# Optimization experiments

Hardware: AMD Instinct MI355X
Metric: run time of the kernel (lower is better)

Reference implementation:

```python
import jax, jax.numpy as jnp
import numpy as np

GROUPS = 32
EPS = 1e-5


def group_norm(x, scale, bias):
    # x: [b, v, t, s, f]; normalize per (b,v,t) sample over (channels_in_group, s)
    b, v, t, s, f = x.shape
    xg = x.reshape(b, v, t, s, GROUPS, f // GROUPS)
    mean = xg.mean(axis=(3, 5), keepdims=True)
    var = xg.var(axis=(3, 5), keepdims=True)
    xn = ((xg - mean) * jax.lax.rsqrt(var + EPS)).reshape(b, v, t, s, f)
    return xn * scale + bias


def nh_conv(x, adjc, W, b):
    # x: [b,v,t,s,f_in]; adjc: [s, k]; W: [k, f_in, f_out]; b: [f_out]
    x_nh = x[:, :, :, adjc, :]                      # [b,v,t,s,k,f_in]
    return jnp.einsum('bvtskf,kfo->bvtso', x_nh, W) + b


def setup_inputs() -> dict:
    key = jax.random.key(0)
    ks = jax.random.split(key, 12)
    B, V, T, S, F_IN, F_OUT, K = 1, 2, 2, 12288, 128, 256, 9
    x = jax.random.normal(ks[0], (B, V, T, S, F_IN), dtype=jnp.float32)
    adjc = jax.random.randint(ks[1], (S, K), 0, S, dtype=jnp.int32)
    gn1_scale = jnp.ones((F_IN,), jnp.float32)
    gn1_bias = jnp.zeros((F_IN,), jnp.float32)
    gn2_scale = jnp.ones((F_OUT,), jnp.float32)
    gn2_bias = jnp.zeros((F_OUT,), jnp.float32)
    W_skip = jax.random.normal(ks[2], (F_IN, F_OUT), jnp.float32) / np.sqrt(F_IN)
    b_skip = jnp.zeros((F_OUT,), jnp.float32)
    W1 = jax.random.normal(ks[3], (K, F_IN, F_OUT), jnp.float32) / np.sqrt(K * F_IN)
    b1 = jnp.zeros((F_OUT,), jnp.float32)
    W2 = jax.random.normal(ks[4], (K, F_OUT, F_OUT), jnp.float32) / np.sqrt(K * F_OUT)
    b2 = jnp.zeros((F_OUT,), jnp.float32)
    return dict(x=x, adjc=adjc, gn1_scale=gn1_scale, gn1_bias=gn1_bias,
                gn2_scale=gn2_scale, gn2_bias=gn2_bias, W_skip=W_skip, b_skip=b_skip,
                W1=W1, b1=b1, W2=W2, b2=b2)


def reference(x, gn1_scale, gn1_bias, gn2_scale, gn2_bias, W_skip, b_skip,
              W1, b1, W2, b2, adjc):
    # skip_layer: ProjLayer with zoom_diff=0 -> plain Linear in->out
    x_res = jnp.einsum('bvtsf,fo->bvtso', x, W_skip) + b_skip
    # norm1 + SiLU (updownconv is Identity when zooms match and in==in feats)
    h = jax.nn.silu(group_norm(x, gn1_scale, gn1_bias))
    # conv1: neighbor-gather linear [k, f_in] -> f_out
    h = nh_conv(h, adjc, W1, b1)
    # emb_layer = Identity; norm2 + SiLU
    h = jax.nn.silu(group_norm(h, gn2_scale, gn2_bias))
    # conv2 + residual
    h = nh_conv(h, adjc, W2, b2)
    return h + x_res
```

## Files before the change

kernel.cpp:

```cpp
#include <hip/hip_runtime.h>
#include <hip/hip_bf16.h>

typedef __bf16 bf16_t;
typedef __bf16 bf16x8 __attribute__((ext_vector_type(8)));
typedef float f32x4 __attribute__((ext_vector_type(4)));
typedef int i32x4 __attribute__((ext_vector_type(4)));

#define S_TOT 12288
#define F_IN 128
#define F_OUT 256
#define EPS 1e-5f

static __device__ __forceinline__ float silu_f(float v) {
  return v / (1.0f + __expf(-v));
}

static __device__ __forceinline__ void gll16(const bf16_t* g, bf16_t* l) {
  __builtin_amdgcn_global_load_lds(
      (const __attribute__((address_space(1))) void*)(const void*)g,
      (__attribute__((address_space(3))) void*)(void*)l, 16, 0, 0);
}

__global__ void prep_kernel(const float* __restrict__ W1,
                            const float* __restrict__ W2,
                            const float* __restrict__ Wsk,
                            bf16_t* __restrict__ W1p,
                            bf16_t* __restrict__ W2p,
                            bf16_t* __restrict__ Wsp,
                            const float* __restrict__ x,
                            float* __restrict__ sum1, float* __restrict__ ss1) {
  __shared__ float gs[32], gq[32];
  if (blockIdx.x < 448) {
    int w = blockIdx.x * 4 + (threadIdx.x >> 6);
    int l = threadIdx.x & 63;
    int lo = l & 15, hi = l >> 4;
    const float* src;
    bf16_t* dst;
    int fbase, obase;
    if (w < 576) {
      int k = w >> 6, rem = w & 63, kc = rem >> 4, cb = rem & 15;
      src = W1 + k * 32768;
      dst = W1p + (size_t)w * 512;
      fbase = 32 * kc + 8 * hi; obase = 16 * cb + lo;
    } else if (w < 1728) {
      int idx = w - 576;
      int k = idx >> 7, rem = idx & 127, kc = rem >> 4, cb = rem & 15;
      src = W2 + k * 65536;
      dst = W2p + (size_t)idx * 512;
      fbase = 32 * kc + 8 * hi; obase = 16 * cb + lo;
    } else {
      int idx = w - 1728;
      int kc = idx >> 4, cb = idx & 15;
      src = Wsk;
      dst = Wsp + (size_t)idx * 512;
      fbase = 32 * kc + 8 * hi; obase = 16 * cb + lo;
    }
    bf16x8 v;
#pragma unroll
    for (int j = 0; j < 8; ++j)
      v[j] = (bf16_t)src[(fbase + j) * 256 + obase];
    *(bf16x8*)(dst + l * 8) = v;
  } else {
    int blk = blockIdx.x - 448;
    int vt = blk & 3;
    int s0 = (blk >> 2) * 256;
    int t = threadIdx.x;
    int col = t & 31, ro = t >> 5;
    float s_ = 0.f, q_ = 0.f;
    const f32x4* xp = (const f32x4*)(x + ((size_t)vt * S_TOT + s0) * F_IN);
#pragma unroll 4
    for (int it = 0; it < 32; ++it) {
      f32x4 v = xp[(size_t)(it * 8 + ro) * 32 + col];
      s_ += v[0] + v[1] + v[2] + v[3];
      q_ += v[0]*v[0] + v[1]*v[1] + v[2]*v[2] + v[3]*v[3];
    }
    if (t < 32) { gs[t] = 0.f; gq[t] = 0.f; }
    __syncthreads();
    atomicAdd(&gs[col], s_);
    atomicAdd(&gq[col], q_);
    __syncthreads();
    if (t < 32) {
      atomicAdd(&sum1[vt * 32 + t], gs[t]);
      atomicAdd(&ss1[vt * 32 + t], gq[t]);
    }
  }
}

__global__ void apply_gn1(const float* __restrict__ x,
                          const float* __restrict__ sum1, const float* __restrict__ ss1,
                          const float* __restrict__ gs, const float* __restrict__ gb,
                          bf16_t* __restrict__ h1) {
  size_t base = ((size_t)blockIdx.x * 256 + threadIdx.x) * 8;
  int vt = (int)(base / ((size_t)S_TOT * F_IN));
  int c0 = (int)(base & (F_IN - 1));
  const f32x4* xp = (const f32x4*)(x + base);
  f32x4 v0 = xp[0], v1 = xp[1];
  float N = (float)(S_TOT * 4);
  bf16x8 o;
#pragma unroll
  for (int gi = 0; gi < 2; ++gi) {
    int g = (c0 >> 2) + gi;
    float mean = sum1[vt * 32 + g] / N;
    float var = ss1[vt * 32 + g] / N - mean * mean;
    float r = rsqrtf(var + EPS);
    f32x4 v = gi ? v1 : v0;
#pragma unroll
    for (int j = 0; j < 4; ++j) {
      int c = g * 4 + j;
      float a = r * gs[c];
      float b = gb[c] - mean * a;
      o[gi * 4 + j] = (bf16_t)silu_f(v[j] * a + b);
    }
  }
  *(bf16x8*)(h1 + base) = o;
}

__global__ void apply_gn2(bf16_t* __restrict__ h,
                          const float* __restrict__ sum_c, const float* __restrict__ ss_c,
                          const float* __restrict__ gs, const float* __restrict__ gb) {
  size_t base = ((size_t)blockIdx.x * 256 + threadIdx.x) * 8;
  int vt = (int)(base / ((size_t)S_TOT * F_OUT));
  int c0 = (int)(base & (F_OUT - 1));
  int g = c0 >> 3;
  bf16x8 v = *(const bf16x8*)(h + base);
  float sg = 0.f, qg = 0.f;
#pragma unroll
  for (int j = 0; j < 8; ++j) {
    sg += sum_c[vt * 256 + g * 8 + j];
    qg += ss_c[vt * 256 + g * 8 + j];
  }
  float N = (float)(S_TOT * 8);
  float mean = sg / N;
  float var = qg / N - mean * mean;
  float r = rsqrtf(var + EPS);
  bf16x8 o;
#pragma unroll
  for (int j = 0; j < 8; ++j) {
    int c = g * 8 + j;
    float a = r * gs[c];
    float b = gb[c] - mean * a;
    o[j] = (bf16_t)silu_f((float)v[j] * a + b);
  }
  *(bf16x8*)(h + base) = o;
}

template<int RE, int NSUB, bool XSK>
__global__ __launch_bounds__(256, 2) void conv_kernel(
    const bf16_t* __restrict__ hsrc, const bf16_t* __restrict__ Wp,
    const bf16_t* __restrict__ Wsp, const float* __restrict__ x,
    const int* __restrict__ adjc, const float* __restrict__ bias,
    const float* __restrict__ biask, bf16_t* __restrict__ outb,
    float* __restrict__ outf, float* __restrict__ sum_c, float* __restrict__ ss_c) {
  const int tid = threadIdx.x;
  const int wv = tid >> 6, l = tid & 63;
  const int lo = l & 15, hi = l >> 4;
  const int nw = wv;

  int swz = ((blockIdx.x & 7) << 6) + (blockIdx.x >> 3);
  int vt = swz >> 7;
  int sblk = swz & 127;
  int s0 = sblk * 96;

  __shared__ int adjs[864];
  __shared__ bf16_t ab[3][4096];

  for (int i = tid; i < 864; i += 256) adjs[i] = adjc[s0 * 9 + i];
  __syncthreads();

  const bf16_t* hb = hsrc + (size_t)vt * ((size_t)S_TOT * RE);
  constexpr int TPK = RE / 32;
  constexpr int NMAIN = XSK ? (NSUB - 4) : NSUB;

  auto stageA = [&](int buf, int s) {
    int tap = s / TPK, chunk = s - tap * TPK;
    {
      int j = wv;
      int row = j * 16 + (l >> 2);
      int segs = (l & 3) ^ ((row >> 1) & 3);
      const bf16_t* g = hb + (size_t)adjs[row * 9 + tap] * RE + chunk * 32 + segs * 8;
      gll16(g, &ab[buf][j * 512]);
    }
    if (wv < 2) {
      int j = 4 + wv;
      int row = j * 16 + (l >> 2);
      int segs = (l & 3) ^ ((row >> 1) & 3);
      const bf16_t* g = hb + (size_t)adjs[row * 9 + tap] * RE + chunk * 32 + segs * 8;
      gll16(g, &ab[buf][j * 512]);
    } else {
      gll16(Wp + l * 8, &ab[buf][(4 + wv) * 512]);
    }
  };

  auto asmB = [&](i32x4* dst, const bf16_t* wsrc, int kcg) {
    const bf16_t* p = wsrc + (size_t)kcg * 8192 + nw * 2048 + l * 8;
    asm volatile(
        "global_load_dwordx4 %0, %4, off\n\t"
        "global_load_dwordx4 %1, %4, off offset:1024\n\t"
        "global_load_dwordx4 %2, %4, off offset:2048\n\t"
        "global_load_dwordx4 %3, %4, off offset:3072"
        : "=&v"(dst[0]), "=&v"(dst[1]), "=&v"(dst[2]), "=&v"(dst[3])
        : "v"(p));
  };

  auto stageX = [&](int buf, int sx) {
    if (tid < 192) {
      int row = tid >> 1, h = tid & 1;
      const float* xr = x + ((size_t)vt * S_TOT + s0 + row) * F_IN + sx * 32 + h * 16;
      f32x4 xv[4];
#pragma unroll
      for (int i = 0; i < 4; ++i) xv[i] = *(const f32x4*)(xr + i * 4);
#pragma unroll
      for (int i = 0; i < 2; ++i) {
        bf16x8 w;
#pragma unroll
        for (int jj = 0; jj < 4; ++jj) {
          w[jj] = (bf16_t)xv[2 * i][jj];
          w[4 + jj] = (bf16_t)xv[2 * i + 1][jj];
        }
        int seg = 2 * h + i;
        *(bf16x8*)(&ab[buf][row * 32 + ((seg ^ ((row >> 1) & 3)) << 3)]) = w;
      }
    }
  };

  f32x4 acc[6][4] = {};
  auto compute = [&](int buf, const i32x4* bv) {
    bf16x8 afr[6];
#pragma unroll
    for (int mi = 0; mi < 6; ++mi) {
      int rr = mi * 16 + lo;
      afr[mi] = *(const bf16x8*)(&ab[buf][rr * 32 + ((hi ^ ((rr >> 1) & 3)) << 3)]);
    }
    __builtin_amdgcn_s_setprio(1);
#pragma unroll
    for (int mi = 0; mi < 6; ++mi)
#pragma unroll
      for (int ni = 0; ni < 4; ++ni)
        acc[mi][ni] = __builtin_amdgcn_mfma_f32_16x16x32_bf16(
            afr[mi], __builtin_bit_cast(bf16x8, bv[ni]), acc[mi][ni], 0, 0, 0);
    __builtin_amdgcn_s_setprio(0);
  };

  i32x4 b0[4], b1[4];
  stageA(0, 0);
  stageA(1, 1);
  asmB(b0, Wp, 0);
  int bcur3 = 0, bstg3 = 2;

  for (int s = 0; s < NMAIN - 2; s += 2) {
    asm volatile("s_waitcnt vmcnt(6)" ::: "memory");
    __builtin_amdgcn_s_barrier();
    __builtin_amdgcn_sched_barrier(0);
    stageA(bstg3, s + 2);
    asmB(b1, Wp, s + 1);
    asm volatile("s_waitcnt vmcnt(6)" ::: "memory");
    __builtin_amdgcn_sched_barrier(0);
    compute(bcur3, b0);
    bcur3 = (bcur3 == 2) ? 0 : bcur3 + 1;
    bstg3 = (bstg3 == 2) ? 0 : bstg3 + 1;
    asm volatile("s_waitcnt vmcnt(6)" ::: "memory");
    __builtin_amdgcn_s_barrier();
    __builtin_amdgcn_sched_barrier(0);
    stageA(bstg3, s + 3);
    asmB(b0, Wp, s + 2);
    asm volatile("s_waitcnt vmcnt(6)" ::: "memory");
    __builtin_amdgcn_sched_barrier(0);
    compute(bcur3, b1);
    bcur3 = (bcur3 == 2) ? 0 : bcur3 + 1;
    bstg3 = (bstg3 == 2) ? 0 : bstg3 + 1;
  }
  asm volatile("s_waitcnt vmcnt(6)" ::: "memory");
  __builtin_amdgcn_s_barrier();
  __builtin_amdgcn_sched_barrier(0);
  asmB(b1, Wp, NMAIN - 1);
  asm volatile("s_waitcnt vmcnt(4)" ::: "memory");
  __builtin_amdgcn_sched_barrier(0);
  compute(bcur3, b0);
  bcur3 = (bcur3 == 2) ? 0 : bcur3 + 1;
  asm volatile("s_waitcnt vmcnt(4)" ::: "memory");
  __builtin_amdgcn_s_barrier();
  __builtin_amdgcn_sched_barrier(0);
  asm volatile("s_waitcnt vmcnt(0)" ::: "memory");
  __builtin_amdgcn_sched_barrier(0);
  compute(bcur3, b1);

  if (XSK) {
#pragma unroll
    for (int sx = 0; sx < 4; ++sx) {
      int tb = sx & 1;
      __syncthreads();
      stageX(tb, sx);
      if (sx & 1) asmB(b1, Wsp, sx); else asmB(b0, Wsp, sx);
      asm volatile("s_waitcnt vmcnt(0)" ::: "memory");
      __syncthreads();
      __builtin_amdgcn_sched_barrier(0);
      compute(tb, (sx & 1) ? (const i32x4*)b1 : (const i32x4*)b0);
    }
  }

  if (!XSK) {
    bf16_t* ob = outb + ((size_t)vt * S_TOT + s0) * 256;
#pragma unroll
    for (int ni = 0; ni < 4; ++ni) {
      int o = nw * 64 + ni * 16 + lo;
      float bv = bias[o];
      float s_ = 0.f, q_ = 0.f;
#pragma unroll
      for (int mi = 0; mi < 6; ++mi)
#pragma unroll
        for (int r2 = 0; r2 < 4; ++r2) {
          int srow = mi * 16 + hi * 4 + r2;
          float v = acc[mi][ni][r2] + bv;
          ob[(size_t)srow * 256 + o] = (bf16_t)v;
          s_ += v; q_ += v * v;
        }
      s_ += __shfl_xor(s_, 16); s_ += __shfl_xor(s_, 32);
      q_ += __shfl_xor(q_, 16); q_ += __shfl_xor(q_, 32);
      if (hi == 0) {
        atomicAdd(&sum_c[vt * 256 + o], s_);
        atomicAdd(&ss_c[vt * 256 + o], q_);
      }
    }
  } else {
    float* of = outf + ((size_t)vt * S_TOT + s0) * 256;
#pragma unroll
    for (int ni = 0; ni < 4; ++ni) {
      int o = nw * 64 + ni * 16 + lo;
      float bv = bias[o] + biask[o];
#pragma unroll
      for (int mi = 0; mi < 6; ++mi)
#pragma unroll
        for (int r2 = 0; r2 < 4; ++r2) {
          int srow = mi * 16 + hi * 4 + r2;
          of[(size_t)srow * 256 + o] = acc[mi][ni][r2] + bv;
        }
    }
  }
}

extern "C" void kernel_launch(void* const* d_in, const int* in_sizes, int n_in,
                              void* d_out, int out_size, void* d_ws, size_t ws_size,
                              hipStream_t stream) {
  const float* x      = (const float*)d_in[0];
  const int*   adjc   = (const int*)d_in[1];
  const float* gn1_s  = (const float*)d_in[2];
  const float* gn1_b  = (const float*)d_in[3];
  const float* gn2_s  = (const float*)d_in[4];
  const float* gn2_b  = (const float*)d_in[5];
  const float* W_skip = (const float*)d_in[6];
  const float* b_skip = (const float*)d_in[7];
  const float* W1     = (const float*)d_in[8];
  const float* b1     = (const float*)d_in[9];
  const float* W2     = (const float*)d_in[10];
  const float* b2     = (const float*)d_in[11];
  float* out = (float*)d_out;

  float* sum1  = (float*)d_ws;
  float* ss1   = sum1 + 128;
  float* sum_c = ss1 + 128;
  float* ss_c  = sum_c + 1024;
  float* pad   = ss_c + 1024;
  bf16_t* W1p  = (bf16_t*)(pad + 3072);
  bf16_t* W2p  = W1p + 294912;
  bf16_t* Wsp  = W2p + 589824;
  bf16_t* h1   = Wsp + 32768;
  bf16_t* out1 = h1 + 6291456;

  hipMemsetAsync(sum1, 0, (128 + 128 + 1024 + 1024) * sizeof(float), stream);
  prep_kernel<<<640, 256, 0, stream>>>(W1, W2, W_skip, W1p, W2p, Wsp, x, sum1, ss1);
  apply_gn1<<<3072, 256, 0, stream>>>(x, sum1, ss1, gn1_s, gn1_b, h1);
  conv_kernel<128, 36, false><<<512, 256, 0, stream>>>(
      h1, W1p, nullptr, nullptr, adjc, b1, nullptr, out1, nullptr, sum_c, ss_c);
  apply_gn2<<<6144, 256, 0, stream>>>(out1, sum_c, ss_c, gn2_s, gn2_b);
  conv_kernel<256, 76, true><<<512, 256, 0, stream>>>(
      out1, W2p, Wsp, x, adjc, b2, b_skip, nullptr, out, nullptr, nullptr);
}
```

Baseline: 152.2 us.

## Reorder K-loop to tap-major chunks and tighten gather/weight pipeline waits

Weight prepacking now orders sub-steps as chunk-major over taps, so consecutive pipeline steps gather different neighbor taps at the same feature chunk. Tap and chunk are tracked incrementally instead of divided. The main loop issues the next weight fragment load before the barrier and removes the second vmcnt wait per half-step, letting the gather, weight load and MFMA overlap more. This risks subtle ordering hazards if the wait counts no longer match the outstanding loads.

```diff
diff --git a/kernel.cpp b/kernel.cpp
--- a/kernel.cpp
+++ b/kernel.cpp
@@ -38,16 +38,18 @@
     bf16_t* dst;
     int fbase, obase;
     if (w < 576) {
-      int k = w >> 6, rem = w & 63, kc = rem >> 4, cb = rem & 15;
-      src = W1 + k * 32768;
+      int kcg = w >> 4, cb = w & 15;
+      int tap = kcg % 9, chunk = kcg / 9;
+      src = W1 + tap * 32768;
       dst = W1p + (size_t)w * 512;
-      fbase = 32 * kc + 8 * hi; obase = 16 * cb + lo;
+      fbase = 32 * chunk + 8 * hi; obase = 16 * cb + lo;
     } else if (w < 1728) {
       int idx = w - 576;
-      int k = idx >> 7, rem = idx & 127, kc = rem >> 4, cb = rem & 15;
-      src = W2 + k * 65536;
+      int kcg = idx >> 4, cb = idx & 15;
+      int tap = kcg % 9, chunk = kcg / 9;
+      src = W2 + tap * 65536;
       dst = W2p + (size_t)idx * 512;
-      fbase = 32 * kc + 8 * hi; obase = 16 * cb + lo;
+      fbase = 32 * chunk + 8 * hi; obase = 16 * cb + lo;
     } else {
       int idx = w - 1728;
       int kc = idx >> 4, cb = idx & 15;
@@ -168,11 +170,9 @@
   __syncthreads();
 
   const bf16_t* hb = hsrc + (size_t)vt * ((size_t)S_TOT * RE);
-  constexpr int TPK = RE / 32;
   constexpr int NMAIN = XSK ? (NSUB - 4) : NSUB;
 
-  auto stageA = [&](int buf, int s) {
-    int tap = s / TPK, chunk = s - tap * TPK;
+  auto stageA = [&](int buf, int tap, int chunk) {
     {
       int j = wv;
       int row = j * 16 + (l >> 2);
@@ -242,45 +242,40 @@
   };
 
   i32x4 b0[4], b1[4];
-  stageA(0, 0);
-  stageA(1, 1);
+  stageA(0, 0, 0);
   asmB(b0, Wp, 0);
+  stageA(1, 1, 0);
   int bcur3 = 0, bstg3 = 2;
+  int t2 = 2, c2 = 0;
 
   for (int s = 0; s < NMAIN - 2; s += 2) {
+    asmB(b1, Wp, s + 1);
     asm volatile("s_waitcnt vmcnt(6)" ::: "memory");
     __builtin_amdgcn_s_barrier();
     __builtin_amdgcn_sched_barrier(0);
-    stageA(bstg3, s + 2);
-    asmB(b1, Wp, s + 1);
-    asm volatile("s_waitcnt vmcnt(6)" ::: "memory");
-    __builtin_amdgcn_sched_barrier(0);
+    stageA(bstg3, t2, c2);
+    if (++t2 == 9) { t2 = 0; ++c2; }
     compute(bcur3, b0);
     bcur3 = (bcur3 == 2) ? 0 : bcur3 + 1;
     bstg3 = (bstg3 == 2) ? 0 : bstg3 + 1;
+    asmB(b0, Wp, s + 2);
     asm volatile("s_waitcnt vmcnt(6)" ::: "memory");
     __builtin_amdgcn_s_barrier();
     __builtin_amdgcn_sched_barrier(0);
-    stageA(bstg3, s + 3);
-    asmB(b0, Wp, s + 2);
-    asm volatile("s_waitcnt vmcnt(6)" ::: "memory");
-    __builtin_amdgcn_sched_barrier(0);
+    stageA(bstg3, t2, c2);
+    if (++t2 == 9) { t2 = 0; ++c2; }
     compute(bcur3, b1);
     bcur3 = (bcur3 == 2) ? 0 : bcur3 + 1;
     bstg3 = (bstg3 == 2) ? 0 : bstg3 + 1;
   }
+  asmB(b1, Wp, NMAIN - 1);
   asm volatile("s_waitcnt vmcnt(6)" ::: "memory");
   __builtin_amdgcn_s_barrier();
   __builtin_amdgcn_sched_barrier(0);
-  asmB(b1, Wp, NMAIN - 1);
-  asm volatile("s_waitcnt vmcnt(4)" ::: "memory");
-  __builtin_amdgcn_sched_barrier(0);
   compute(bcur3, b0);
   bcur3 = (bcur3 == 2) ? 0 : bcur3 + 1;
-  asm volatile("s_waitcnt vmcnt(4)" ::: "memory");
+  asm volatile("s_waitcnt vmcnt(0)" ::: "memory");
   __builtin_amdgcn_s_barrier();
-  __builtin_amdgcn_sched_barrier(0);
-  asm volatile("s_waitcnt vmcnt(0)" ::: "memory");
   __builtin_amdgcn_sched_barrier(0);
   compute(bcur3, b1);
 
```

After: 144.3 us. -5.2%, faster.
